# Kernel optimization log

Measured on AMD Instinct MI355X. Metric: run time of the kernel, lower is better.

Reference implementation:

```python
import jax, jax.numpy as jnp
import numpy as np

B, T, D = 4, 4096, 1024
H = 16
DK = D // H
EPS = 1e-6


def _phi(x):
    return jax.nn.elu(x) + 1.0


def setup_inputs() -> dict:
    key = jax.random.key(0)
    ks = jax.random.split(key, 9)
    s = 1.0 / np.sqrt(D)
    return {
        "x": jax.random.normal(ks[0], (B, T, D), dtype=jnp.float32),
        "Wq": jax.random.uniform(ks[1], (D, D), jnp.float32, -s, s),
        "bq": jax.random.uniform(ks[2], (D,), jnp.float32, -s, s),
        "Wk": jax.random.uniform(ks[3], (D, D), jnp.float32, -s, s),
        "bk": jax.random.uniform(ks[4], (D,), jnp.float32, -s, s),
        "Wv": jax.random.uniform(ks[5], (D, D), jnp.float32, -s, s),
        "bv": jax.random.uniform(ks[6], (D,), jnp.float32, -s, s),
        "Wo": jax.random.uniform(ks[7], (D, D), jnp.float32, -s, s),
        "bo": jax.random.uniform(ks[8], (D,), jnp.float32, -s, s),
    }


def reference(x, Wq, bq, Wk, bk, Wv, bv, Wo, bo):
    Bq, Tq, _ = x.shape

    def heads(y):  # [B,T,D] -> [B,H,T,DK]
        return y.reshape(Bq, Tq, H, DK).transpose(0, 2, 1, 3)

    q = _phi(heads(x @ Wq.T + bq))
    k = _phi(heads(x @ Wk.T + bk))
    v = heads(x @ Wv.T + bv)

    # associative KV summary: [B,H,DK,DK]
    kv = jnp.einsum("bhtd,bhtm->bhdm", k, v)
    # normalizer: q . (sum_t k + eps), then +eps, reciprocal
    z = 1.0 / (jnp.einsum("bhtd,bhd->bht", q, k.sum(axis=2) + EPS) + EPS)
    out = jnp.einsum("bhtd,bhdm,bht->bhtm", q, kv, z)

    out = out.transpose(0, 2, 1, 3).reshape(Bq, Tq, -1)  # [B,T,D]
    return out @ Wo.T + bo
```

## Files before the change

kernel.cpp:

```cpp
#include <hip/hip_runtime.h>
#include <cstdint>
#include <cstddef>

typedef unsigned short u16;
typedef __bf16 bf16x8 __attribute__((ext_vector_type(8)));
typedef float  f32x4  __attribute__((ext_vector_type(4)));
typedef u16    u16x8v __attribute__((ext_vector_type(8)));
typedef u16    u16x4  __attribute__((ext_vector_type(4)));

#define EPS 1e-6f

__device__ __forceinline__ u16 f2bf(float f) {
  union { float f; unsigned int u; } v; v.f = f;
  unsigned int u = v.u + 0x7FFFu + ((v.u >> 16) & 1u);
  return (u16)(u >> 16);
}
__device__ __forceinline__ float bf2f(u16 h) {
  union { unsigned int u; float f; } v; v.u = ((unsigned int)h) << 16;
  return v.f;
}
__device__ __forceinline__ void async16(const void* g, void* l) {
  __builtin_amdgcn_global_load_lds(
      (const __attribute__((address_space(1))) void*)g,
      (__attribute__((address_space(3))) void*)l, 16, 0, 0);
}

__global__ __launch_bounds__(256) void cvt_bf16_kernel(
    const float* __restrict__ in, u16* __restrict__ out, int n8) {
  int i = blockIdx.x * 256 + threadIdx.x;
  if (i >= n8) return;
  const float4* p = (const float4*)in;
  float4 a = p[2 * (size_t)i], b = p[2 * (size_t)i + 1];
  u16x8v o;
  o[0] = f2bf(a.x); o[1] = f2bf(a.y); o[2] = f2bf(a.z); o[3] = f2bf(a.w);
  o[4] = f2bf(b.x); o[5] = f2bf(b.y); o[6] = f2bf(b.z); o[7] = f2bf(b.w);
  *(u16x8v*)(out + 8 * (size_t)i) = o;
}

__global__ __launch_bounds__(256) void cvt_w_kernel(
    const float* __restrict__ w0, const float* __restrict__ w1,
    const float* __restrict__ w2, const float* __restrict__ w3,
    u16* __restrict__ o0, u16* __restrict__ o1,
    u16* __restrict__ o2, u16* __restrict__ o3) {
  const int gb = blockIdx.x;
  const float* in = (gb < 512) ? w0 : (gb < 1024) ? w1 : (gb < 1536) ? w2 : w3;
  u16* out = (gb < 512) ? o0 : (gb < 1024) ? o1 : (gb < 1536) ? o2 : o3;
  const int i = (gb & 511) * 256 + threadIdx.x;
  const float4* p = (const float4*)in;
  float4 a = p[2 * (size_t)i], b = p[2 * (size_t)i + 1];
  u16x8v o;
  o[0] = f2bf(a.x); o[1] = f2bf(a.y); o[2] = f2bf(a.z); o[3] = f2bf(a.w);
  o[4] = f2bf(b.x); o[5] = f2bf(b.y); o[6] = f2bf(b.z); o[7] = f2bf(b.w);
  *(u16x8v*)(out + 8 * (size_t)i) = o;
}

template <int MODE>
__global__ __launch_bounds__(512) void gemm4p(
    const u16* __restrict__ A, const u16* __restrict__ Bw,
    const float* __restrict__ bias0, const float* __restrict__ bias1,
    const float* __restrict__ bias2,
    u16* __restrict__ O0, u16* __restrict__ O1, u16* __restrict__ O2,
    float* __restrict__ Of, int K) {
  __shared__ u16 sA[2][256 * 64];
  __shared__ u16 sB[2][256 * 64];

  const int tid = threadIdx.x, wave = tid >> 6, lane = tid & 63;
  const int bm = blockIdx.x * 256, bn = blockIdx.y * 256;
  const int wmh = (wave >> 2) * 64;
  const int wq  = (wave & 3) * 32;
  const int l15 = lane & 15, l4 = lane >> 4, l7 = lane & 7;

  f32x4 acc[8][4] = {};

  const int trow = tid >> 3;
  const int sch8 = ((tid & 7) ^ (trow & 7)) * 8;

#define STG_A(buf, qm, s, kt)                                                 \
  async16(A + (size_t)(bm + (s)*128 + (qm)*64 + trow) * K + (kt) + sch8,      \
          &sA[buf][(((qm)*128 + (s)*64) + wave * 8) * 64])
#define STG_B(buf, qn, s, kt)                                                 \
  async16(Bw + (size_t)(bn + ((s)*2 + (trow >> 5)) * 64 + (qn)*32 +           \
                        (trow & 31)) * K + (kt) + sch8,                       \
          &sB[buf][(((qn)*128 + (s)*64) + wave * 8) * 64])

  bf16x8 af[4][2], bq[4][2];

#define RD_A(buf, qm)                                                         \
  _Pragma("unroll") for (int m = 0; m < 4; m++)                               \
    _Pragma("unroll") for (int kk = 0; kk < 2; kk++)                          \
      af[m][kk] = *(const bf16x8*)&sA[buf][((qm)*128 + wmh + m * 16 + l15) * 64 \
                                           + ((kk * 4 + l4) ^ l7) * 8];
#define RD_B(buf)                                                             \
  _Pragma("unroll") for (int nf = 0; nf < 4; nf++)                            \
    _Pragma("unroll") for (int kk = 0; kk < 2; kk++)                          \
      bq[nf][kk] = *(const bf16x8*)&sB[buf][((nf >> 1) * 128 + wq +           \
                                            (nf & 1) * 16 + l15) * 64 +       \
                                           ((kk * 4 + l4) ^ l7) * 8];

#define WAITV(n) asm volatile("s_waitcnt vmcnt(" #n ")" ::: "memory")

#define PH_EXEC(qm, NW)                                                       \
  __builtin_amdgcn_s_barrier();                                               \
  asm volatile("s_waitcnt lgkmcnt(0)" ::: "memory");                          \
  __builtin_amdgcn_sched_barrier(0);                                          \
  __builtin_amdgcn_s_setprio(1);                                              \
  _Pragma("unroll") for (int kk = 0; kk < 2; kk++)                            \
    _Pragma("unroll") for (int m = 0; m < 4; m++)                             \
      _Pragma("unroll") for (int nf = 0; nf < 4; nf++)                        \
        acc[(qm)*4 + m][nf] = __builtin_amdgcn_mfma_f32_16x16x32_bf16(        \
            af[m][kk], bq[nf][kk], acc[(qm)*4 + m][nf], 0, 0, 0);             \
  __builtin_amdgcn_s_setprio(0);                                              \
  WAITV(NW);                                                                  \
  __builtin_amdgcn_s_barrier();                                               \
  asm volatile("" ::: "memory");

#define ITER_BODY(kO, kE2, kO2, hasT2, hasT3, W0, W1, W2, W3)                 \
                                          \
  RD_B(0); RD_A(0, 0);                                                        \
  STG_A(1, 1, 0, kO); STG_A(1, 1, 1, kO);               \
  PH_EXEC(0, W0);                                                             \
                                                          \
  RD_A(0, 1);                                                                 \
  if (hasT2) {                                                                \
    STG_B(0, 0, 0, kE2); STG_B(0, 0, 1, kE2);                                 \
    STG_B(0, 1, 0, kE2); STG_B(0, 1, 1, kE2);                       \
    STG_A(0, 0, 0, kE2); STG_A(0, 0, 1, kE2);                      \
  }                                                                           \
  PH_EXEC(1, W1);                                                             \
                                          \
  RD_B(1); RD_A(1, 0);                                                        \
  if (hasT2) { STG_A(0, 1, 0, kE2); STG_A(0, 1, 1, kE2); }         \
  PH_EXEC(0, W2);                                                             \
                                                          \
  RD_A(1, 1);                                                                 \
  if (hasT3) {                                                                \
    STG_B(1, 0, 0, kO2); STG_B(1, 0, 1, kO2);                                 \
    STG_B(1, 1, 0, kO2); STG_B(1, 1, 1, kO2);                       \
    STG_A(1, 0, 0, kO2); STG_A(1, 0, 1, kO2);                      \
  }                                                                           \
  PH_EXEC(1, W3);

  STG_B(0, 0, 0, 0);  STG_B(0, 0, 1, 0);  STG_B(0, 1, 0, 0);  STG_B(0, 1, 1, 0);
  STG_A(0, 0, 0, 0);  STG_A(0, 0, 1, 0);
  STG_A(0, 1, 0, 0);  STG_A(0, 1, 1, 0);
  STG_B(1, 0, 0, 64); STG_B(1, 0, 1, 64); STG_B(1, 1, 0, 64); STG_B(1, 1, 1, 64);
  STG_A(1, 0, 0, 64); STG_A(1, 0, 1, 64);
  WAITV(6);
  __builtin_amdgcn_s_barrier();
  asm volatile("" ::: "memory");

  const int NT = K >> 6;
  const int NI = NT >> 1;
  for (int i = 0; i < NI - 1; ++i) {
    const int kO  = (2 * i + 1) * 64;
    const int kE2 = (2 * i + 2) * 64;
    const int kO2 = (2 * i + 3) * 64;
    ITER_BODY(kO, kE2, kO2, true, true, 8, 8, 8, 8);
  }
  {
    const int kO = (NT - 1) * 64;
    ITER_BODY(kO, 0, 0, false, false, 8, 2, 0, 0);
  }
#undef STG_A
#undef STG_B
#undef RD_A
#undef RD_B
#undef WAITV
#undef PH_EXEC
#undef ITER_BODY

  const int wm = wmh * 2;
  const int wn = (wave & 3) * 64;
  const int r0 = l4 * 4, cc = l15;
  if constexpr (MODE == 1) {
    const int mat = blockIdx.y >> 2;
    u16* outp = (mat == 0) ? O0 : (mat == 1) ? O1 : O2;
    const float* bias = (mat == 0) ? bias0 : (mat == 1) ? bias1 : bias2;
    const int act = (mat < 2);
    const int colb = (blockIdx.y & 3) * 256;
    float bvv[4];
#pragma unroll
    for (int ni = 0; ni < 4; ni++) bvv[ni] = bias[colb + wn + ni * 16 + cc];
#pragma unroll
    for (int mi = 0; mi < 8; mi++) {
#pragma unroll
      for (int j = 0; j < 4; j++) {
        const int row = bm + wm + mi * 16 + r0 + j;
#pragma unroll
        for (int ni = 0; ni < 4; ni++) {
          const int col = colb + wn + ni * 16 + cc;
          float val = acc[mi][ni][j] + bvv[ni];
          if (act) val = (val > 0.f) ? (val + 1.f) : __expf(val);
          outp[(size_t)row * 1024 + col] = f2bf(val);
        }
      }
    }
  } else {
    float bvv[4];
#pragma unroll
    for (int ni = 0; ni < 4; ni++) bvv[ni] = bias0[bn + wn + ni * 16 + cc];
#pragma unroll
    for (int mi = 0; mi < 8; mi++) {
#pragma unroll
      for (int j = 0; j < 4; j++) {
        const int row = bm + wm + mi * 16 + r0 + j;
#pragma unroll
        for (int ni = 0; ni < 4; ni++) {
          const int col = bn + wn + ni * 16 + cc;
          Of[(size_t)row * 1024 + col] = acc[mi][ni][j] + bvv[ni];
        }
      }
    }
  }
}

__global__ __launch_bounds__(256) void kv_mfma_kernel(
    const u16* __restrict__ Kb, const u16* __restrict__ Vb,
    float* __restrict__ kv, float* __restrict__ ksum) {
  const int bh = blockIdx.y;
  const int chunk = blockIdx.x;
  const int b = bh >> 4, h = bh & 15;
  const int tid = threadIdx.x, wave = tid >> 6, lane = tid & 63;

  __shared__ u16 sKT[64 * 64];
  __shared__ u16 sVT[64 * 64];

  f32x4 acc[4] = {};
  f32x4 accs[4] = {};

  union { u16x8v u; bf16x8 b; } uo;
#pragma unroll
  for (int e = 0; e < 8; e++) uo.u[e] = 0x3F80;
  const bf16x8 ones = uo.b;

  const int half = tid >> 7;
  const int j    = tid & 127;
  const int tg   = j >> 3;
  const int dg   = j & 7;
  const u16* src = half ? Vb : Kb;
  u16* dst = half ? sVT : sKT;
  const int colb = (4 * tg + 8 * dg) & 63;

  const size_t rowBase = (size_t)b * 4096 + (size_t)chunk * 512;
  const size_t gbase = (rowBase + 4 * tg) * 1024 + (size_t)h * 64 + dg * 8;

  u16x8v pre[2][4];
#pragma unroll
  for (int s = 0; s < 4; s++)
    pre[0][s] = *(const u16x8v*)(src + gbase + (size_t)s * 1024);

#pragma unroll
  for (int st = 0; st < 8; st++) {
    const int cb = st & 1;
    __syncthreads();
#pragma unroll
    for (int e = 0; e < 8; e++) {
      u16x4 w;
      w[0] = pre[cb][0][e]; w[1] = pre[cb][1][e];
      w[2] = pre[cb][2][e]; w[3] = pre[cb][3][e];
      *(u16x4*)&dst[(dg * 8 + e) * 64 + colb] = w;
    }
    if (st + 1 < 8) {
      const size_t nb = gbase + (size_t)(st + 1) * 64 * 1024;
#pragma unroll
      for (int s = 0; s < 4; s++)
        pre[cb ^ 1][s] = *(const u16x8v*)(src + nb + (size_t)s * 1024);
    }
    __syncthreads();

#pragma unroll
    for (int kst = 0; kst < 2; kst++) {
      const int q8 = kst * 32 + (lane >> 4) * 8;
      bf16x8 bfrag;
      {
        const int rr = wave * 16 + (lane & 15);
        const int c = (q8 + 8 * (rr >> 3)) & 63;
        bfrag = *(const bf16x8*)&sVT[rr * 64 + c];
      }
#pragma unroll
      for (int i = 0; i < 4; i++) {
        const int rr = i * 16 + (lane & 15);
        const int c = (q8 + 8 * (rr >> 3)) & 63;
        const bf16x8 afrag = *(const bf16x8*)&sKT[rr * 64 + c];
        acc[i] = __builtin_amdgcn_mfma_f32_16x16x32_bf16(afrag, bfrag, acc[i], 0, 0, 0);
        if (wave == 0)
          accs[i] = __builtin_amdgcn_mfma_f32_16x16x32_bf16(afrag, ones, accs[i], 0, 0, 0);
      }
    }
  }

  const int r0 = (lane >> 4) * 4, cc = lane & 15;
  float* kvp = kv + (size_t)bh * 4096;
#pragma unroll
  for (int i = 0; i < 4; i++)
#pragma unroll
    for (int jj = 0; jj < 4; jj++)
      atomicAdd(&kvp[(size_t)(i * 16 + r0 + jj) * 64 + wave * 16 + cc], acc[i][jj]);
  if (wave == 0 && cc == 0) {
#pragma unroll
    for (int i = 0; i < 4; i++)
#pragma unroll
      for (int jj = 0; jj < 4; jj++)
        atomicAdd(&ksum[(size_t)bh * 64 + i * 16 + r0 + jj], accs[i][jj]);
  }
}

#define QST 80
__global__ __launch_bounds__(256) void attn_apply_kernel(
    const u16* __restrict__ Qb, const float* __restrict__ kv,
    const float* __restrict__ ksum, u16* __restrict__ attn) {
  const int bh = blockIdx.y;
  const int tt = blockIdx.x;
  const int b = bh >> 4, h = bh & 15;
  const int tid = threadIdx.x, wave = tid >> 6, lane = tid & 63;

  __shared__ u16 skvT[64 * QST];
  __shared__ u16 sq[64 * QST];
  __shared__ float sz[64];
  __shared__ float sks[64];

  if (tid < 64) sks[tid] = ksum[(size_t)bh * 64 + tid] + EPS;

  const float* kvp = kv + (size_t)bh * 4096;
  for (int i = tid; i < 4096; i += 256) {
    const int dd = i >> 6, mm = i & 63;
    skvT[mm * QST + dd] = f2bf(kvp[i]);
  }
  const size_t qbase = ((size_t)b * 4096 + (size_t)tt * 64) * 1024 + h * 64;
  for (int i = tid; i < 4096; i += 256) {
    const int r = i >> 6, dd = i & 63;
    sq[r * QST + dd] = Qb[qbase + (size_t)r * 1024 + dd];
  }
  __syncthreads();

  if (tid < 64) {
    float za = 0.f;
#pragma unroll
    for (int j = 0; j < 64; j++) {
      const int dd = (j + tid) & 63;
      za += bf2f(sq[tid * QST + dd]) * sks[dd];
    }
    sz[tid] = 1.f / (za + EPS);
  }
  __syncthreads();

  f32x4 acc[4] = {};
#pragma unroll
  for (int ks2 = 0; ks2 < 2; ks2++) {
    const bf16x8 a = *(const bf16x8*)&sq[(wave * 16 + (lane & 15)) * QST + ks2 * 32 + (lane >> 4) * 8];
#pragma unroll
    for (int ni = 0; ni < 4; ni++) {
      const bf16x8 bv = *(const bf16x8*)&skvT[(ni * 16 + (lane & 15)) * QST + ks2 * 32 + (lane >> 4) * 8];
      acc[ni] = __builtin_amdgcn_mfma_f32_16x16x32_bf16(a, bv, acc[ni], 0, 0, 0);
    }
  }

  const int r0 = (lane >> 4) * 4, cc = lane & 15;
#pragma unroll
  for (int ni = 0; ni < 4; ni++) {
#pragma unroll
    for (int j = 0; j < 4; j++) {
      const int r = wave * 16 + r0 + j;
      const int c = ni * 16 + cc;
      const float val = acc[ni][j] * sz[r];
      attn[qbase + (size_t)r * 1024 + c] = f2bf(val);
    }
  }
}

extern "C" void kernel_launch(void* const* d_in, const int* in_sizes, int n_in,
                              void* d_out, int out_size, void* d_ws, size_t ws_size,
                              hipStream_t stream) {
  (void)in_sizes; (void)n_in; (void)out_size; (void)ws_size;
  const float* x  = (const float*)d_in[0];
  const float* Wq = (const float*)d_in[1];
  const float* bq = (const float*)d_in[2];
  const float* Wk = (const float*)d_in[3];
  const float* bk = (const float*)d_in[4];
  const float* Wv = (const float*)d_in[5];
  const float* bv = (const float*)d_in[6];
  const float* Wo = (const float*)d_in[7];
  const float* bo = (const float*)d_in[8];

  char* ws = (char*)d_ws;
  u16* xb    = (u16*)ws;  ws += 33554432;
  u16* wqkvb = (u16*)ws;  ws += 6291456;
  u16* wob   = (u16*)ws;  ws += 2097152;
  u16* Vb    = (u16*)ws;  ws += 33554432;
  u16* attn  = (u16*)ws;  ws += 33554432;
  float* kvb  = (float*)ws; ws += 1048576;
  float* ksum = (float*)ws; ws += 16384;

  u16* Qb = (u16*)d_out;
  u16* Kb = Qb + 16777216;

  hipMemsetAsync(kvb, 0, 1048576 + 16384, stream);

  cvt_bf16_kernel<<<8192, 256, 0, stream>>>(x, xb, 2097152);
  cvt_w_kernel<<<2048, 256, 0, stream>>>(Wq, Wk, Wv, Wo,
                                         wqkvb, wqkvb + 1048576, wqkvb + 2097152, wob);

  gemm4p<1><<<dim3(64, 12), 512, 0, stream>>>(
      xb, wqkvb, bq, bk, bv, Qb, Kb, Vb, nullptr, 1024);

  kv_mfma_kernel<<<dim3(8, 64), dim3(256), 0, stream>>>(Kb, Vb, kvb, ksum);
  attn_apply_kernel<<<dim3(64, 64), dim3(256), 0, stream>>>(Qb, kvb, ksum, attn);

  gemm4p<0><<<dim3(64, 4), 512, 0, stream>>>(
      attn, wob, bo, nullptr, nullptr, nullptr, nullptr, nullptr,
      (float*)d_out, 1024);
}
```

Measured before the change: 319.7 us.

## Split GEMM main loop into eight quadrant phases with finer-grained prefetch

Restructures the bf16 GEMM inner loop from four half-tile phases into eight quarter-tile phases (2 M halves x 2 N halves), each doing 8 MFMAs per k-step. Global-to-LDS async loads are spread more evenly across the phases, and the vmcnt waits are retuned. The aim is to overlap the LDS-bound loads with MFMA work more smoothly and to cut B-fragment register pressure. In exchange there are twice as many barriers per iteration, and the buffer-reuse ordering is more fragile.

```diff
diff --git a/kernel.cpp b/kernel.cpp
--- a/kernel.cpp
+++ b/kernel.cpp
@@ -55,7 +55,7 @@
 }
 
 template <int MODE>
-__global__ __launch_bounds__(512) void gemm4p(
+__global__ __launch_bounds__(512) void gemm8g(
     const u16* __restrict__ A, const u16* __restrict__ Bw,
     const float* __restrict__ bias0, const float* __restrict__ bias1,
     const float* __restrict__ bias2,
@@ -83,91 +83,100 @@
                         (trow & 31)) * K + (kt) + sch8,                       \
           &sB[buf][(((qn)*128 + (s)*64) + wave * 8) * 64])
 
-  bf16x8 af[4][2], bq[4][2];
+  bf16x8 af[4][2], bq[2][2];
 
 #define RD_A(buf, qm)                                                         \
   _Pragma("unroll") for (int m = 0; m < 4; m++)                               \
     _Pragma("unroll") for (int kk = 0; kk < 2; kk++)                          \
       af[m][kk] = *(const bf16x8*)&sA[buf][((qm)*128 + wmh + m * 16 + l15) * 64 \
                                            + ((kk * 4 + l4) ^ l7) * 8];
-#define RD_B(buf)                                                             \
-  _Pragma("unroll") for (int nf = 0; nf < 4; nf++)                            \
+#define RD_B(buf, qn)                                                         \
+  _Pragma("unroll") for (int f = 0; f < 2; f++)                               \
     _Pragma("unroll") for (int kk = 0; kk < 2; kk++)                          \
-      bq[nf][kk] = *(const bf16x8*)&sB[buf][((nf >> 1) * 128 + wq +           \
-                                            (nf & 1) * 16 + l15) * 64 +       \
-                                           ((kk * 4 + l4) ^ l7) * 8];
-
-#define WAITV(n) asm volatile("s_waitcnt vmcnt(" #n ")" ::: "memory")
-
-#define PH_EXEC(qm, NW)                                                       \
+      bq[f][kk] = *(const bf16x8*)&sB[buf][((qn)*128 + wq + f * 16 + l15) * 64 \
+                                           + ((kk * 4 + l4) ^ l7) * 8];
+
+#define WAITV_(n) asm volatile("s_waitcnt vmcnt(" #n ")" ::: "memory")
+#define WAITV(n) WAITV_(n)
+
+#define PH(qm, qn, W)                                                         \
   __builtin_amdgcn_s_barrier();                                               \
   asm volatile("s_waitcnt lgkmcnt(0)" ::: "memory");                          \
   __builtin_amdgcn_sched_barrier(0);                                          \
   __builtin_amdgcn_s_setprio(1);                                              \
   _Pragma("unroll") for (int kk = 0; kk < 2; kk++)                            \
     _Pragma("unroll") for (int m = 0; m < 4; m++)                             \
-      _Pragma("unroll") for (int nf = 0; nf < 4; nf++)                        \
-        acc[(qm)*4 + m][nf] = __builtin_amdgcn_mfma_f32_16x16x32_bf16(        \
-            af[m][kk], bq[nf][kk], acc[(qm)*4 + m][nf], 0, 0, 0);             \
+      _Pragma("unroll") for (int n = 0; n < 2; n++)                           \
+        acc[(qm)*4 + m][(qn)*2 + n] = __builtin_amdgcn_mfma_f32_16x16x32_bf16(\
+            af[m][kk], bq[n][kk], acc[(qm)*4 + m][(qn)*2 + n], 0, 0, 0);      \
   __builtin_amdgcn_s_setprio(0);                                              \
-  WAITV(NW);                                                                  \
+  WAITV(W);                                                                   \
   __builtin_amdgcn_s_barrier();                                               \
   asm volatile("" ::: "memory");
 
-#define ITER_BODY(kO, kE2, kO2, hasT2, hasT3, W0, W1, W2, W3)                 \
-                                          \
-  RD_B(0); RD_A(0, 0);                                                        \
-  STG_A(1, 1, 0, kO); STG_A(1, 1, 1, kO);               \
-  PH_EXEC(0, W0);                                                             \
+#define ITER8(kO, kE2, kO2, FULL, W0, W1, W2, W3, W4, W5, W6, W7)             \
+                                                   \
+  RD_A(0, 0); RD_B(0, 0);                                                     \
+  STG_B(1, 0, 0, kO); STG_B(1, 0, 1, kO);                \
+  PH(0, 0, W0);                                                               \
+                                                          \
+  RD_B(0, 1);                                                                 \
+  if (FULL) { STG_A(0, 0, 0, kE2); STG_A(0, 0, 1, kE2); }          \
+  PH(0, 1, W1);                                                               \
                                                           \
   RD_A(0, 1);                                                                 \
-  if (hasT2) {                                                                \
-    STG_B(0, 0, 0, kE2); STG_B(0, 0, 1, kE2);                                 \
-    STG_B(0, 1, 0, kE2); STG_B(0, 1, 1, kE2);                       \
-    STG_A(0, 0, 0, kE2); STG_A(0, 0, 1, kE2);                      \
-  }                                                                           \
-  PH_EXEC(1, W1);                                                             \
-                                          \
-  RD_B(1); RD_A(1, 0);                                                        \
-  if (hasT2) { STG_A(0, 1, 0, kE2); STG_A(0, 1, 1, kE2); }         \
-  PH_EXEC(0, W2);                                                             \
+  if (FULL) { STG_B(0, 1, 0, kE2); STG_B(0, 1, 1, kE2); }          \
+  PH(1, 1, W2);                                                               \
+                                                          \
+  RD_B(0, 0);                                                                 \
+  if (FULL) { STG_A(0, 1, 0, kE2); STG_A(0, 1, 1, kE2); }          \
+  PH(1, 0, W3);                                                               \
+                                                   \
+  RD_A(1, 0); RD_B(1, 0);                                                     \
+  if (FULL) { STG_B(0, 0, 0, kE2); STG_B(0, 0, 1, kE2); }          \
+  PH(0, 0, W4);                                                               \
+                                                          \
+  RD_B(1, 1);                                                                 \
+  if (FULL) { STG_A(1, 0, 0, kO2); STG_A(1, 0, 1, kO2); }          \
+  PH(0, 1, W5);                                                               \
                                                           \
   RD_A(1, 1);                                                                 \
-  if (hasT3) {                                                                \
-    STG_B(1, 0, 0, kO2); STG_B(1, 0, 1, kO2);                                 \
-    STG_B(1, 1, 0, kO2); STG_B(1, 1, 1, kO2);                       \
-    STG_A(1, 0, 0, kO2); STG_A(1, 0, 1, kO2);                      \
-  }                                                                           \
-  PH_EXEC(1, W3);
-
-  STG_B(0, 0, 0, 0);  STG_B(0, 0, 1, 0);  STG_B(0, 1, 0, 0);  STG_B(0, 1, 1, 0);
+  if (FULL) { STG_B(1, 1, 0, kO2); STG_B(1, 1, 1, kO2); }          \
+  PH(1, 1, W6);                                                               \
+                                                          \
+  RD_B(1, 0);                                                                 \
+  if (FULL) { STG_A(1, 1, 0, kO2); STG_A(1, 1, 1, kO2); }          \
+  PH(1, 0, W7);
+
   STG_A(0, 0, 0, 0);  STG_A(0, 0, 1, 0);
+  STG_B(0, 0, 0, 0);  STG_B(0, 0, 1, 0);
+  STG_B(0, 1, 0, 0);  STG_B(0, 1, 1, 0);
   STG_A(0, 1, 0, 0);  STG_A(0, 1, 1, 0);
-  STG_B(1, 0, 0, 64); STG_B(1, 0, 1, 64); STG_B(1, 1, 0, 64); STG_B(1, 1, 1, 64);
   STG_A(1, 0, 0, 64); STG_A(1, 0, 1, 64);
-  WAITV(6);
+  STG_B(1, 1, 0, 64); STG_B(1, 1, 1, 64);
+  STG_A(1, 1, 0, 64); STG_A(1, 1, 1, 64);
+  WAITV(10);
   __builtin_amdgcn_s_barrier();
   asm volatile("" ::: "memory");
 
   const int NT = K >> 6;
   const int NI = NT >> 1;
-  for (int i = 0; i < NI - 1; ++i) {
+  ITER8(64, 128, 192, true, 10, 10, 12, 12, 12, 12, 12, 12);
+  for (int i = 1; i < NI - 1; ++i) {
     const int kO  = (2 * i + 1) * 64;
     const int kE2 = (2 * i + 2) * 64;
     const int kO2 = (2 * i + 3) * 64;
-    ITER_BODY(kO, kE2, kO2, true, true, 8, 8, 8, 8);
-  }
-  {
-    const int kO = (NT - 1) * 64;
-    ITER_BODY(kO, 0, 0, false, false, 8, 2, 0, 0);
-  }
+    ITER8(kO, kE2, kO2, true, 12, 12, 12, 12, 12, 12, 12, 12);
+  }
+  ITER8((NT - 1) * 64, 0, 0, false, 12, 10, 8, 6, 4, 2, 0, 0);
 #undef STG_A
 #undef STG_B
 #undef RD_A
 #undef RD_B
 #undef WAITV
-#undef PH_EXEC
-#undef ITER_BODY
+#undef WAITV_
+#undef PH
+#undef ITER8
 
   const int wm = wmh * 2;
   const int wn = (wave & 3) * 64;
@@ -400,13 +409,13 @@
   cvt_w_kernel<<<2048, 256, 0, stream>>>(Wq, Wk, Wv, Wo,
                                          wqkvb, wqkvb + 1048576, wqkvb + 2097152, wob);
 
-  gemm4p<1><<<dim3(64, 12), 512, 0, stream>>>(
+  gemm8g<1><<<dim3(64, 12), 512, 0, stream>>>(
       xb, wqkvb, bq, bk, bv, Qb, Kb, Vb, nullptr, 1024);
 
   kv_mfma_kernel<<<dim3(8, 64), dim3(256), 0, stream>>>(Kb, Vb, kvb, ksum);
   attn_apply_kernel<<<dim3(64, 64), dim3(256), 0, stream>>>(Qb, kvb, ksum, attn);
 
-  gemm4p<0><<<dim3(64, 4), 512, 0, stream>>>(
+  gemm8g<0><<<dim3(64, 4), 512, 0, stream>>>(
       attn, wob, bo, nullptr, nullptr, nullptr, nullptr, nullptr,
       (float*)d_out, 1024);
 }
```

Result: slower. 327.2 us (+2.3%).
